# Kernel tuning notes

Measured on AMD Instinct MI355X. Metric: run time of the kernel, lower is better.

Reference implementation:

```python
import jax, jax.numpy as jnp
import numpy as np

S, B, E, H = 512, 128, 256, 256  # seq_len (nodes), num_samples, embb_dim, hidd_dim
CLIP = 10.0


def setup_inputs() -> dict:
    key = jax.random.key(0)
    ks = jax.random.split(key, 12)
    sc = 1.0 / np.sqrt(H)
    rn = lambda k, shape, s: (jax.random.normal(k, shape, dtype=jnp.float32) * s)
    x = rn(ks[0], (S, E), 1.0)
    # Gumbel noise for deterministic multinomial (Gumbel-argmax) sampling
    u = jax.random.uniform(ks[1], (S, B, S), minval=1e-6, maxval=1.0 - 1e-6)
    gumbel = -jnp.log(-jnp.log(u))
    return {
        "x": x,
        "gumbel": gumbel,
        "W_ih": rn(ks[2], (4 * H, E), sc),
        "W_hh": rn(ks[3], (4 * H, H), sc),
        "b_ih": jnp.zeros((4 * H,), jnp.float32),
        "b_hh": jnp.zeros((4 * H,), jnp.float32),
        "Wa_dec": rn(ks[4], (H, H), sc),
        "Wa_enc": rn(ks[5], (H, H), sc),
        "b_a": jnp.zeros((H,), jnp.float32),
        "v": rn(ks[6], (H,), sc),
        "init_dec": jnp.zeros((E,), jnp.float32),
        "num_samples": B,
    }


def _pointer_decode(x, gumbel, W_ih, W_hh, b_ih, b_hh, Wa_dec, Wa_enc, b_a, v,
                    init_dec, num_samples):
    Sn = x.shape[0]
    Bn = num_samples
    Hh = W_hh.shape[1]
    # encoder part of additive attention, computed once: [S, H]
    enc_proj = x @ Wa_enc.T + b_a

    h0 = jnp.zeros((Bn, Hh), x.dtype)
    c0 = jnp.zeros((Bn, Hh), x.dtype)
    dec0 = jnp.broadcast_to(init_dec, (Bn, init_dec.shape[0]))
    mask0 = jnp.ones((Bn, Sn), bool)
    lps0 = jnp.zeros((Bn,), x.dtype)
    ar = jnp.arange(Bn)

    def step(carry, g):
        h, c, di, m, lps = carry
        # single-layer LSTM cell (torch gate order: i, f, g, o)
        gates = di @ W_ih.T + b_ih + h @ W_hh.T + b_hh
        i_, f_, g_, o_ = jnp.split(gates, 4, axis=-1)
        c = jax.nn.sigmoid(f_) * c + jax.nn.sigmoid(i_) * jnp.tanh(g_)
        h = jax.nn.sigmoid(o_) * jnp.tanh(c)
        # additive attention: tanh(W [dec; enc] + b) . v, with logit clipping
        energy = jnp.tanh((h @ Wa_dec.T)[:, None, :] + enc_proj[None, :, :])  # [B,S,H]
        logits = CLIP * jnp.tanh(energy @ v)  # [B,S]
        logits = jnp.where(m, logits, -jnp.inf)
        lp = jax.nn.log_softmax(logits, axis=1)
        # multinomial sample via Gumbel-argmax over unmasked probs
        sel = jnp.argmax(lp + g, axis=1)  # [B]
        lps = lps + lp[ar, sel]
        di = x[sel]  # next decoder input = embedding of chosen node
        m = m.at[ar, sel].set(False)  # mask out chosen node
        return (h, c, di, m, lps), sel

    (_, _, _, _, log_probs_sum), sels = jax.lax.scan(
        step, (h0, c0, dec0, mask0, lps0), gumbel)
    predicted_mappings = sels.T  # [B, S]
    return predicted_mappings, log_probs_sum


def reference(x, gumbel, W_ih, W_hh, b_ih, b_hh, Wa_dec, Wa_enc, b_a, v,
              init_dec, num_samples):
    return _pointer_decode(x, gumbel, W_ih, W_hh, b_ih, b_hh, Wa_dec, Wa_enc,
                           b_a, v, init_dec, num_samples)
```

## Files before the change

kernel.cpp:

```cpp
#include <hip/hip_runtime.h>
#include <math.h>

#define SN 512
#define BN 128
#define HN 256
#define NSLICE 16
#define NGRP   16

#define B_EPT    ((size_t)0)
#define B_XPROJ  ((size_t)1048576)
#define B_IPROJ  ((size_t)5242880)
#define B_BIAS   ((size_t)5251072)
#define B_WIHT   ((size_t)5259264)
#define B_XT     ((size_t)6307840)
#define B_EX     ((size_t)6832128)
#define PAR_STRIDE 131072
#define EX_SLOTS  (2*PAR_STRIDE)

#define L_PB    0
#define L_PP3   36864
#define L_PF    73728
#define L_VLD   110592
#define L_HF    112640
#define L_HWF   129280
#define L_XPRO  145920
#define L_MASK  150016
#define L_CL    152064
#define L_BIAS  153088
#define L_SEL   153600
#define SMEM_TOTAL 153664

typedef double v2d __attribute__((ext_vector_type(2)));

#define TAGC 0x9E3779B97F4A7C15ULL
__device__ __forceinline__ long long d2ll(double d) { return __double_as_longlong(d); }

__device__ __forceinline__ double rcp64(double d) {
    double r;
    asm("v_rcp_f64 %0, %1" : "=v"(r) : "v"(d));
    r = __builtin_fma(__builtin_fma(-d, r, 1.0), r, r);
    r = __builtin_fma(__builtin_fma(-d, r, 1.0), r, r);
    return r;
}
__device__ __forceinline__ double rcp64f(double d) {
    double r;
    asm("v_rcp_f64 %0, %1" : "=v"(r) : "v"(d));
    r = __builtin_fma(__builtin_fma(-d, r, 1.0), r, r);
    return r;
}

__device__ __forceinline__ double exp2n(double t) {
    t = fmax(t, -1000.0);
    double n = __builtin_rint(t);
    double z = (t - n) * 0.69314718055994530942;
    double p = 2.5052108385441718775e-8;
    p = __builtin_fma(p, z, 2.7557319223985892511e-7);
    p = __builtin_fma(p, z, 2.7557319223985890653e-6);
    p = __builtin_fma(p, z, 2.4801587301587301566e-5);
    p = __builtin_fma(p, z, 1.9841269841269841253e-4);
    p = __builtin_fma(p, z, 1.3888888888888889419e-3);
    p = __builtin_fma(p, z, 8.3333333333333332177e-3);
    p = __builtin_fma(p, z, 4.1666666666666664354e-2);
    p = __builtin_fma(p, z, 1.6666666666666666574e-1);
    p = __builtin_fma(p, z, 0.5);
    p = __builtin_fma(p, z, 1.0);
    p = __builtin_fma(p, z, 1.0);
    long long ni = (long long)(int)n;
    return __longlong_as_double(__double_as_longlong(p) + (ni << 52));
}
__device__ __forceinline__ double tanh64(double x) {
    double a = fabs(x);
    double e = exp2n(a * -2.8853900817779268147);
    double r = rcp64(1.0 + e);
    return copysign((1.0 - e) * r, x);
}
__device__ __forceinline__ double sigmoid64(double g) {
    double a = fabs(g);
    double e = exp2n(a * -1.4426950408889634074);
    double r = rcp64(1.0 + e);
    double num = (g >= 0.0) ? 1.0 : e;
    return num * r;
}

__device__ __forceinline__ void pub16(double2* p, double v, unsigned long long tg) {
    v2d t2;
    t2.x = v;
    t2.y = __longlong_as_double(d2ll(v) ^ (long long)tg);
    asm volatile("global_store_dwordx4 %0, %1, off sc0 sc1" :: "v"(p), "v"(t2) : "memory");
}
__device__ __forceinline__ void gath2(const double2* p, unsigned long long tg,
                                      double* o0, double* o1) {
    v2d a, b;
    for (;;) {
        asm volatile("global_load_dwordx4 %0, %2, off sc0 sc1\n\t"
                     "global_load_dwordx4 %1, %2, off offset:16 sc0 sc1\n\t"
                     "s_waitcnt vmcnt(0)"
                     : "=&v"(a), "=&v"(b) : "v"(p) : "memory");
        bool ok = ((d2ll(a.x) ^ d2ll(a.y)) == (long long)tg) &
                  ((d2ll(b.x) ^ d2ll(b.y)) == (long long)tg);
        if (ok) break;
        __builtin_amdgcn_s_sleep(2);
    }
    *o0 = a.x; *o1 = b.x;
}

__global__ __launch_bounds__(256) void k_init_transpose(
    const float* __restrict__ Wih, const float* __restrict__ bih,
    const float* __restrict__ bhh, const float* __restrict__ x,
    float* __restrict__ ws)
{
    char* wsb = (char*)ws;
    float*  wiht = (float*)(wsb + B_WIHT);
    float*  xt   = (float*)(wsb + B_XT);
    double* bias = (double*)(wsb + B_BIAS);
    double2* ex  = (double2*)(wsb + B_EX);
    int i = blockIdx.x * 256 + threadIdx.x;
    if (i < 262144) {
        int e = i >> 10, r = i & 1023;
        wiht[i] = Wih[(size_t)r * 256 + e];
    } else if (i < 393216) {
        int j = i - 262144; int e = j >> 9, s = j & 511;
        xt[j] = x[(size_t)s * 256 + e];
    } else if (i < 394240) {
        int j = i - 393216;
        bias[j] = (double)bih[j] + (double)bhh[j];
    } else if (i < 394240 + EX_SLOTS) {
        double2 z; z.x = 0.0; z.y = 0.0;
        ex[i - 394240] = z;
    }
}

__global__ __launch_bounds__(512) void k_init_proj(
    const float* __restrict__ x, const float* __restrict__ Wae,
    const float* __restrict__ ba, const float* __restrict__ idec,
    float* __restrict__ ws)
{
    char* wsb = (char*)ws;
    const float* wiht = (const float*)(wsb + B_WIHT);
    const float* xt   = (const float*)(wsb + B_XT);
    double* ept   = (double*)(wsb + B_EPT);
    double* xproj = (double*)(wsb + B_XPROJ);
    double* iproj = (double*)(wsb + B_IPROJ);
    int blk = blockIdx.x, tid = threadIdx.x;
    if (blk < 256) {
        int k = blk, s = tid;
        double a = 0.0;
        for (int e = 0; e < 256; ++e)
            a += (double)Wae[(size_t)k * 256 + e] * (double)xt[(size_t)e * 512 + s];
        ept[(size_t)k * 512 + s] = tanh((double)ba[k] + a);
    } else if (blk < 256 + 1024) {
        int idx = blk - 256;
        int s = idx >> 1;
        int r = (idx & 1) * 512 + tid;
        double a = 0.0;
        for (int e = 0; e < 256; ++e)
            a += (double)x[(size_t)s * 256 + e] * (double)wiht[(size_t)e * 1024 + r];
        xproj[(size_t)s * 1024 + r] = a;
    } else {
        int r = (blk - 1280) * 512 + tid;
        double a = 0.0;
        for (int e = 0; e < 256; ++e)
            a += (double)idec[e] * (double)wiht[(size_t)e * 1024 + r];
        iproj[r] = a;
    }
}

__global__ __launch_bounds__(512, 2) void k_decode(
    const float* __restrict__ gmb, const float* __restrict__ vvec,
    const float* __restrict__ Whh, const float* __restrict__ Wad,
    float* __restrict__ ws, float* __restrict__ out)
{
    extern __shared__ char smem[];
    double* pb   = (double*)(smem + L_PB);
    double* pp3  = (double*)(smem + L_PP3);
    double* pf   = (double*)(smem + L_PF);
    double* vLd  = (double*)(smem + L_VLD);
    double* hf   = (double*)(smem + L_HF);
    double* hwf  = (double*)(smem + L_HWF);
    double* xpro = (double*)(smem + L_XPRO);
    double* mask = (double*)(smem + L_MASK);
    double* c_l  = (double*)(smem + L_CL);
    double* bias_l = (double*)(smem + L_BIAS);
    int*    selA = (int*)(smem + L_SEL);

    const int tid = threadIdx.x;
    const int g = blockIdx.x & 15;
    const int q = blockIdx.x >> 4;

    char* wsb = (char*)ws;
    const double* eptG   = (const double*)(wsb + B_EPT);
    const double* xprojG = (const double*)(wsb + B_XPROJ);
    const double* biasG  = (const double*)(wsb + B_BIAS);
    const double* iprojG = (const double*)(wsb + B_IPROJ);
    double2* exB = (double2*)(wsb + B_EX);

    for (int i = tid; i < 256; i += 512) vLd[i] = (double)vvec[i];
    if (tid < 64) bias_l[tid] = biasG[((tid >> 4) << 8) + q * 16 + (tid & 15)];
    for (int i = tid; i < 256; i += 512) mask[i] = 0.0;
    for (int i = tid; i < 128; i += 512) c_l[i] = 0.0;
    for (int i = tid; i < 2080; i += 512) { hf[i] = 0.0; hwf[i] = 0.0; }
    {
        int sl = tid >> 6, rl = tid & 63;
        int rg = ((rl >> 4) << 8) + q * 16 + (rl & 15);
        xpro[sl * 64 + rl] = iprojG[rg];
    }

    const int w = tid >> 6, lane = tid & 63;
    const int kc4 = tid >> 5, ss = tid & 31;

    double ev[16];
    #pragma unroll
    for (int kk = 0; kk < 16; ++kk)
        ev[kk] = eptG[(size_t)(kc4 * 16 + kk) * 512 + q * 32 + ss];
    const int rg1 = ((lane >> 4) << 8) + q * 16 + (lane & 15);
    const int kbase = w * 32;
    float wreg[32];
    {
        const float4* wrow = (const float4*)(Whh + (size_t)rg1 * 256 + kbase);
        #pragma unroll
        for (int j = 0; j < 8; ++j) {
            float4 v4 = wrow[j];
            wreg[4 * j + 0] = v4.x; wreg[4 * j + 1] = v4.y;
            wreg[4 * j + 2] = v4.z; wreg[4 * j + 3] = v4.w;
        }
    }
    float w3[8];
    {
        const float* wr3 = Wad + (size_t)(q * 16 + (tid & 15)) * 256 + (tid >> 4) * 8;
        #pragma unroll
        for (int kk = 0; kk < 8; ++kk) w3[kk] = wr3[kk];
    }
    __syncthreads();

    double lps = 0.0;

    for (int t = 0; t < SN; ++t) {
        const unsigned long long tg = (unsigned long long)(t + 2) * TAGC;
        double2* parB   = exB + (size_t)(t & 1) * PAR_STRIDE;
        double2* hexP   = parB + (size_t)g * 2048;
        double2* waexP  = parB + 32768 + (size_t)g * 2048;
        double2* lexP   = parB + 65536 + (size_t)g * 4096;

        float gv8[8];
        {
            const float* growW = gmb + (size_t)t * (BN * SN) + (size_t)(g * 8 + w) * SN;
            #pragma unroll
            for (int j = 0; j < 8; ++j)
                gv8[j] = __builtin_nontemporal_load(growW + lane + 64 * j);
        }

        #pragma unroll
        for (int slin = 0; slin < 4; ++slin) {
            int sl = slin;
            double a0 = 0.0, a1 = 0.0, a2 = 0.0, a3 = 0.0;
            #pragma unroll
            for (int g4 = 0; g4 < 8; ++g4) {
                const double* hp = hf + sl * 260 + kbase + 4 * g4;
                double2 hA = *(const double2*)(hp);
                double2 hB = *(const double2*)(hp + 2);
                a0 += (double)wreg[4 * g4 + 0] * hA.x;
                a1 += (double)wreg[4 * g4 + 1] * hA.y;
                a2 += (double)wreg[4 * g4 + 2] * hB.x;
                a3 += (double)wreg[4 * g4 + 3] * hB.y;
            }
            pb[w * 576 + lane * 9 + sl] = ((a0 + a1) + (a2 + a3));
        }
        __syncthreads();

        if (w == 0) {
            int jl = lane & 15, slin = lane >> 4;
            int sl = slin;
            double gvv[4];
            #pragma unroll
            for (int gate = 0; gate < 4; ++gate) {
                int rl = gate * 16 + jl;
                double p0 = pb[0 * 576 + rl * 9 + sl], p1 = pb[1 * 576 + rl * 9 + sl];
                double p2 = pb[2 * 576 + rl * 9 + sl], p3 = pb[3 * 576 + rl * 9 + sl];
                double p4 = pb[4 * 576 + rl * 9 + sl], p5 = pb[5 * 576 + rl * 9 + sl];
                double p6 = pb[6 * 576 + rl * 9 + sl], p7 = pb[7 * 576 + rl * 9 + sl];
                double s8 = ((p0 + p1) + (p2 + p3)) + ((p4 + p5) + (p6 + p7));
                gvv[gate] = bias_l[rl] + xpro[sl * 64 + rl] + s8;
            }
            double si = sigmoid64(gvv[0]);
            double sf = sigmoid64(gvv[1]);
            double so = sigmoid64(gvv[3]);
            double cf = sf * c_l[jl * 8 + sl] + si * tanh64(gvv[2]);
            double hn = so * tanh64(cf);
            c_l[jl * 8 + sl] = cf;
            pub16(&hexP[sl * 256 + q * 16 + jl], hn, tg);
        }

        #pragma unroll
        for (int slin = 0; slin < 4; ++slin) {
            int sl = 4 + slin;
            double a0 = 0.0, a1 = 0.0, a2 = 0.0, a3 = 0.0;
            #pragma unroll
            for (int g4 = 0; g4 < 8; ++g4) {
                const double* hp = hf + sl * 260 + kbase + 4 * g4;
                double2 hA = *(const double2*)(hp);
                double2 hB = *(const double2*)(hp + 2);
                a0 += (double)wreg[4 * g4 + 0] * hA.x;
                a1 += (double)wreg[4 * g4 + 1] * hA.y;
                a2 += (double)wreg[4 * g4 + 2] * hB.x;
                a3 += (double)wreg[4 * g4 + 3] * hB.y;
            }
            pb[w * 576 + lane * 9 + sl] = ((a0 + a1) + (a2 + a3));
        }
        __syncthreads();

        if (w == 1) {
            int jl = lane & 15, slin = lane >> 4;
            int sl = 4 + slin;
            double gvv[4];
            #pragma unroll
            for (int gate = 0; gate < 4; ++gate) {
                int rl = gate * 16 + jl;
                double p0 = pb[0 * 576 + rl * 9 + sl], p1 = pb[1 * 576 + rl * 9 + sl];
                double p2 = pb[2 * 576 + rl * 9 + sl], p3 = pb[3 * 576 + rl * 9 + sl];
                double p4 = pb[4 * 576 + rl * 9 + sl], p5 = pb[5 * 576 + rl * 9 + sl];
                double p6 = pb[6 * 576 + rl * 9 + sl], p7 = pb[7 * 576 + rl * 9 + sl];
                double s8 = ((p0 + p1) + (p2 + p3)) + ((p4 + p5) + (p6 + p7));
                gvv[gate] = bias_l[rl] + xpro[sl * 64 + rl] + s8;
            }
            double si = sigmoid64(gvv[0]);
            double sf = sigmoid64(gvv[1]);
            double so = sigmoid64(gvv[3]);
            double cf = sf * c_l[jl * 8 + sl] + si * tanh64(gvv[2]);
            double hn = so * tanh64(cf);
            c_l[jl * 8 + sl] = cf;
            pub16(&hexP[sl * 256 + q * 16 + jl], hn, tg);
        }

        {
            int sl = lane >> 4;
            int k  = kbase + (lane & 15) * 2;
            gath2(hexP + sl * 256 + k, tg, &hf[sl * 260 + k], &hf[sl * 260 + k + 1]);
        }

        {
            int kc = tid >> 4, rl = tid & 15;
            #pragma unroll
            for (int sl = 0; sl < 4; ++sl) {
                double a = 0.0;
                #pragma unroll
                for (int kk = 0; kk < 8; ++kk)
                    a += (double)w3[kk] * hf[sl * 260 + kc * 8 + kk];
                pp3[kc * 144 + rl * 9 + sl] = a;
            }
        }
        __syncthreads();
        if (w == 2) {
            int rl = lane & 15, slin = lane >> 4;
            int sl = slin;
            double s = 0.0;
            for (int kc = 0; kc < 32; ++kc) s += pp3[kc * 144 + rl * 9 + sl];
            pub16(&waexP[sl * 256 + q * 16 + rl], tanh64(s), tg);
        }

        {
            int sl = 4 + (lane >> 4);
            int k  = kbase + (lane & 15) * 2;
            gath2(hexP + sl * 256 + k, tg, &hf[sl * 260 + k], &hf[sl * 260 + k + 1]);
        }

        {
            int kc = tid >> 4, rl = tid & 15;
            #pragma unroll
            for (int slin = 0; slin < 4; ++slin) {
                int sl = 4 + slin;
                double a = 0.0;
                #pragma unroll
                for (int kk = 0; kk < 8; ++kk)
                    a += (double)w3[kk] * hf[sl * 260 + kc * 8 + kk];
                pp3[kc * 144 + rl * 9 + sl] = a;
            }
        }
        __syncthreads();
        if (w == 3) {
            int rl = lane & 15, slin = lane >> 4;
            int sl = 4 + slin;
            double s = 0.0;
            for (int kc = 0; kc < 32; ++kc) s += pp3[kc * 144 + rl * 9 + sl];
            pub16(&waexP[sl * 256 + q * 16 + rl], tanh64(s), tg);
        }

        {
            int sl = lane >> 4;
            int k  = kbase + (lane & 15) * 2;
            gath2(waexP + sl * 256 + k, tg, &hwf[sl * 260 + k], &hwf[sl * 260 + k + 1]);
        }

        {
            double vd[16];
            #pragma unroll
            for (int kk = 0; kk < 16; ++kk) vd[kk] = vLd[kc4 * 16 + kk];
            #pragma unroll 1
            for (int sl = 0; sl < 4; ++sl) {
                double a = 0.0;
                #pragma unroll
                for (int j = 0; j < 8; ++j) {
                    double2 h2 = *(const double2*)(hwf + sl * 260 + kc4 * 16 + 2 * j);
                    {
                        double Ta = ev[2 * j + 0], Tb = h2.x;
                        double d = __builtin_fma(Ta, Tb, 1.0);
                        double r = rcp64f(d);
                        a = __builtin_fma(vd[2 * j + 0], (Ta + Tb) * r, a);
                    }
                    {
                        double Ta = ev[2 * j + 1], Tb = h2.y;
                        double d = __builtin_fma(Ta, Tb, 1.0);
                        double r = rcp64f(d);
                        a = __builtin_fma(vd[2 * j + 1], (Ta + Tb) * r, a);
                    }
                }
                pf[kc4 * 288 + ss * 9 + sl] = a;
            }
        }
        __syncthreads();
        if (tid < 128) {
            int sA = tid & 31, slin = tid >> 5;
            int sl = slin;
            double u = 0.0;
            for (int kc = 0; kc < 16; ++kc) u += pf[kc * 288 + sA * 9 + sl];
            double lg = 10.0 * tanh64(u);
            pub16(&lexP[sl * 512 + q * 32 + sA], lg + mask[sA * 8 + sl], tg);
        }

        {
            int sl = 4 + (lane >> 4);
            int k  = kbase + (lane & 15) * 2;
            gath2(waexP + sl * 256 + k, tg, &hwf[sl * 260 + k], &hwf[sl * 260 + k + 1]);
        }

        {
            double vd[16];
            #pragma unroll
            for (int kk = 0; kk < 16; ++kk) vd[kk] = vLd[kc4 * 16 + kk];
            #pragma unroll 1
            for (int slin = 0; slin < 4; ++slin) {
                int sl = 4 + slin;
                double a = 0.0;
                #pragma unroll
                for (int j = 0; j < 8; ++j) {
                    double2 h2 = *(const double2*)(hwf + sl * 260 + kc4 * 16 + 2 * j);
                    {
                        double Ta = ev[2 * j + 0], Tb = h2.x;
                        double d = __builtin_fma(Ta, Tb, 1.0);
                        double r = rcp64f(d);
                        a = __builtin_fma(vd[2 * j + 0], (Ta + Tb) * r, a);
                    }
                    {
                        double Ta = ev[2 * j + 1], Tb = h2.y;
                        double d = __builtin_fma(Ta, Tb, 1.0);
                        double r = rcp64f(d);
                        a = __builtin_fma(vd[2 * j + 1], (Ta + Tb) * r, a);
                    }
                }
                pf[kc4 * 288 + ss * 9 + sl] = a;
            }
        }
        __syncthreads();
        if (tid < 128) {
            int sA = tid & 31, slin = tid >> 5;
            int sl = 4 + slin;
            double u = 0.0;
            for (int kc = 0; kc < 16; ++kc) u += pf[kc * 288 + sA * 9 + sl];
            double lg = 10.0 * tanh64(u);
            pub16(&lexP[sl * 512 + q * 32 + sA], lg + mask[sA * 8 + sl], tg);
        }

        {
            const double2* b0 = lexP + (size_t)w * 512 + lane;
            const double2* b1 = b0 + 256;
            double lv[8];
            for (;;) {
                v2d q0, q1, q2, q3, q4, q5, q6, q7;
                asm volatile(
                    "global_load_dwordx4 %0, %8, off sc0 sc1\n\t"
                    "global_load_dwordx4 %1, %8, off offset:1024 sc0 sc1\n\t"
                    "global_load_dwordx4 %2, %8, off offset:2048 sc0 sc1\n\t"
                    "global_load_dwordx4 %3, %8, off offset:3072 sc0 sc1\n\t"
                    "global_load_dwordx4 %4, %9, off sc0 sc1\n\t"
                    "global_load_dwordx4 %5, %9, off offset:1024 sc0 sc1\n\t"
                    "global_load_dwordx4 %6, %9, off offset:2048 sc0 sc1\n\t"
                    "global_load_dwordx4 %7, %9, off offset:3072 sc0 sc1\n\t"
                    "s_waitcnt vmcnt(0)"
                    : "=&v"(q0), "=&v"(q1), "=&v"(q2), "=&v"(q3),
                      "=&v"(q4), "=&v"(q5), "=&v"(q6), "=&v"(q7)
                    : "v"(b0), "v"(b1) : "memory");
                bool ok = ((d2ll(q0.x) ^ d2ll(q0.y)) == (long long)tg) &
                          ((d2ll(q1.x) ^ d2ll(q1.y)) == (long long)tg) &
                          ((d2ll(q2.x) ^ d2ll(q2.y)) == (long long)tg) &
                          ((d2ll(q3.x) ^ d2ll(q3.y)) == (long long)tg) &
                          ((d2ll(q4.x) ^ d2ll(q4.y)) == (long long)tg) &
                          ((d2ll(q5.x) ^ d2ll(q5.y)) == (long long)tg) &
                          ((d2ll(q6.x) ^ d2ll(q6.y)) == (long long)tg) &
                          ((d2ll(q7.x) ^ d2ll(q7.y)) == (long long)tg);
                if (ok) {
                    lv[0] = q0.x; lv[1] = q1.x; lv[2] = q2.x; lv[3] = q3.x;
                    lv[4] = q4.x; lv[5] = q5.x; lv[6] = q6.x; lv[7] = q7.x;
                    break;
                }
                __builtin_amdgcn_s_sleep(2);
            }
            double M = -INFINITY;
            #pragma unroll
            for (int j = 0; j < 8; ++j) M = fmax(M, lv[j]);
            #pragma unroll
            for (int off = 32; off >= 1; off >>= 1) M = fmax(M, __shfl_xor(M, off, 64));
            float se = 0.f;
            #pragma unroll
            for (int j = 0; j < 8; ++j) se += expf((float)(lv[j] - M));
            #pragma unroll
            for (int off = 32; off >= 1; off >>= 1) se += __shfl_xor(se, off, 64);
            float logS = logf(se);
            double best = -INFINITY; int bidx = 0x7fffffff; double bl = 0.0;
            #pragma unroll
            for (int j = 0; j < 8; ++j) {
                int s = lane + 64 * j;
                double cd = lv[j] + (double)gv8[j];
                if (cd > best || (cd == best && s < bidx)) { best = cd; bidx = s; bl = lv[j]; }
            }
            #pragma unroll
            for (int off = 32; off >= 1; off >>= 1) {
                double ob = __shfl_xor(best, off, 64);
                int    oi = __shfl_xor(bidx, off, 64);
                double ol = __shfl_xor(bl, off, 64);
                if (ob > best || (ob == best && oi < bidx)) { best = ob; bidx = oi; bl = ol; }
            }
            lps += (bl - M) - (double)logS;
            if (lane == 0) {
                selA[w] = bidx;
                if (q == 0) out[(size_t)(g * 8 + w) * SN + t] = (float)bidx;
            }
        }
        __syncthreads();
        if (tid < 256) {
            int sA = tid >> 3, sl = tid & 7;
            if (selA[sl] == q * 32 + sA) mask[sA * 8 + sl] = -INFINITY;
        }
        {
            int sl = tid >> 6, rl = tid & 63;
            int rg = ((rl >> 4) << 8) + q * 16 + (rl & 15);
            xpro[sl * 64 + rl] = xprojG[(size_t)selA[sl] * 1024 + rg];
        }
    }
    if (q == 0 && lane == 0) out[(size_t)BN * SN + g * 8 + w] = (float)lps;
}

extern "C" void kernel_launch(void* const* d_in, const int* in_sizes, int n_in,
                              void* d_out, int out_size, void* d_ws, size_t ws_size,
                              hipStream_t stream)
{
    const float* x    = (const float*)d_in[0];
    const float* gmb  = (const float*)d_in[1];
    const float* Wih  = (const float*)d_in[2];
    const float* Whh  = (const float*)d_in[3];
    const float* bih  = (const float*)d_in[4];
    const float* bhh  = (const float*)d_in[5];
    const float* Wad  = (const float*)d_in[6];
    const float* Wae  = (const float*)d_in[7];
    const float* ba   = (const float*)d_in[8];
    const float* vvec = (const float*)d_in[9];
    const float* idec = (const float*)d_in[10];
    float* ws = (float*)d_ws;
    float* out = (float*)d_out;

    hipFuncSetAttribute(reinterpret_cast<const void*>(k_decode),
                        hipFuncAttributeMaxDynamicSharedMemorySize, SMEM_TOTAL);

    hipLaunchKernelGGL(k_init_transpose, dim3(2564), dim3(256), 0, stream,
                       Wih, bih, bhh, x, ws);
    hipLaunchKernelGGL(k_init_proj, dim3(1282), dim3(512), 0, stream,
                       x, Wae, ba, idec, ws);
    hipLaunchKernelGGL(k_decode, dim3(256), dim3(512), SMEM_TOTAL, stream,
                       gmb, vvec, Whh, Wad, ws, out);
}
```

Baseline: 8.885 ms.

## Merge half-batch phases and overlap next-step recurrent matvec with logit exchange

Drops the split of each step into two half-batch passes per stage (LSTM gates, Wa_dec projection, attention energy), so each stage now handles all 8 local samples at once with fewer block barriers and global exchange rounds. The W_hh·h partial products for the next step are now computed right after the logits are published, overlapping the wait on other blocks' logits, and pb is zero-initialised so the first step sees h=0. Spin-wait sleep shrinks to the minimum. The cost is that the old overlap between the two halves is lost, and polling becomes more aggressive.

Result: slower. 9.520 ms (+7.2%).

```diff
diff --git a/kernel.cpp b/kernel.cpp
--- a/kernel.cpp
+++ b/kernel.cpp
@@ -15,7 +15,7 @@
 #define B_XT     ((size_t)6307840)
 #define B_EX     ((size_t)6832128)
 #define PAR_STRIDE 131072
-#define EX_SLOTS  (2*PAR_STRIDE)
+#define EX_TOTAL  (2*PAR_STRIDE)
 
 #define L_PB    0
 #define L_PP3   36864
@@ -96,10 +96,9 @@
                      "global_load_dwordx4 %1, %2, off offset:16 sc0 sc1\n\t"
                      "s_waitcnt vmcnt(0)"
                      : "=&v"(a), "=&v"(b) : "v"(p) : "memory");
-        bool ok = ((d2ll(a.x) ^ d2ll(a.y)) == (long long)tg) &
-                  ((d2ll(b.x) ^ d2ll(b.y)) == (long long)tg);
-        if (ok) break;
-        __builtin_amdgcn_s_sleep(2);
+        if (((d2ll(a.x) ^ d2ll(a.y)) == (long long)tg) &
+            ((d2ll(b.x) ^ d2ll(b.y)) == (long long)tg)) break;
+        __builtin_amdgcn_s_sleep(1);
     }
     *o0 = a.x; *o1 = b.x;
 }
@@ -124,7 +123,7 @@
     } else if (i < 394240) {
         int j = i - 393216;
         bias[j] = (double)bih[j] + (double)bhh[j];
-    } else if (i < 394240 + EX_SLOTS) {
+    } else if (i < 394240 + EX_TOTAL) {
         double2 z; z.x = 0.0; z.y = 0.0;
         ex[i - 394240] = z;
     }
@@ -199,6 +198,7 @@
     for (int i = tid; i < 256; i += 512) mask[i] = 0.0;
     for (int i = tid; i < 128; i += 512) c_l[i] = 0.0;
     for (int i = tid; i < 2080; i += 512) { hf[i] = 0.0; hwf[i] = 0.0; }
+    for (int i = tid; i < 4608; i += 512) pb[i] = 0.0;
     {
         int sl = tid >> 6, rl = tid & 63;
         int rg = ((rl >> 4) << 8) + q * 16 + (rl & 15);
@@ -241,6 +241,8 @@
         double2* waexP  = parB + 32768 + (size_t)g * 2048;
         double2* lexP   = parB + 65536 + (size_t)g * 4096;
 
+        __syncthreads();
+
         float gv8[8];
         {
             const float* growW = gmb + (size_t)t * (BN * SN) + (size_t)(g * 8 + w) * SN;
@@ -249,27 +251,9 @@
                 gv8[j] = __builtin_nontemporal_load(growW + lane + 64 * j);
         }
 
-        #pragma unroll
-        for (int slin = 0; slin < 4; ++slin) {
-            int sl = slin;
-            double a0 = 0.0, a1 = 0.0, a2 = 0.0, a3 = 0.0;
-            #pragma unroll
-            for (int g4 = 0; g4 < 8; ++g4) {
-                const double* hp = hf + sl * 260 + kbase + 4 * g4;
-                double2 hA = *(const double2*)(hp);
-                double2 hB = *(const double2*)(hp + 2);
-                a0 += (double)wreg[4 * g4 + 0] * hA.x;
-                a1 += (double)wreg[4 * g4 + 1] * hA.y;
-                a2 += (double)wreg[4 * g4 + 2] * hB.x;
-                a3 += (double)wreg[4 * g4 + 3] * hB.y;
-            }
-            pb[w * 576 + lane * 9 + sl] = ((a0 + a1) + (a2 + a3));
-        }
-        __syncthreads();
-
-        if (w == 0) {
+        if (w < 2) {
             int jl = lane & 15, slin = lane >> 4;
-            int sl = slin;
+            int sl = w * 4 + slin;
             double gvv[4];
             #pragma unroll
             for (int gate = 0; gate < 4; ++gate) {
@@ -290,57 +274,18 @@
             pub16(&hexP[sl * 256 + q * 16 + jl], hn, tg);
         }
 
-        #pragma unroll
-        for (int slin = 0; slin < 4; ++slin) {
-            int sl = 4 + slin;
-            double a0 = 0.0, a1 = 0.0, a2 = 0.0, a3 = 0.0;
-            #pragma unroll
-            for (int g4 = 0; g4 < 8; ++g4) {
-                const double* hp = hf + sl * 260 + kbase + 4 * g4;
-                double2 hA = *(const double2*)(hp);
-                double2 hB = *(const double2*)(hp + 2);
-                a0 += (double)wreg[4 * g4 + 0] * hA.x;
-                a1 += (double)wreg[4 * g4 + 1] * hA.y;
-                a2 += (double)wreg[4 * g4 + 2] * hB.x;
-                a3 += (double)wreg[4 * g4 + 3] * hB.y;
-            }
-            pb[w * 576 + lane * 9 + sl] = ((a0 + a1) + (a2 + a3));
-        }
-        __syncthreads();
-
-        if (w == 1) {
-            int jl = lane & 15, slin = lane >> 4;
-            int sl = 4 + slin;
-            double gvv[4];
-            #pragma unroll
-            for (int gate = 0; gate < 4; ++gate) {
-                int rl = gate * 16 + jl;
-                double p0 = pb[0 * 576 + rl * 9 + sl], p1 = pb[1 * 576 + rl * 9 + sl];
-                double p2 = pb[2 * 576 + rl * 9 + sl], p3 = pb[3 * 576 + rl * 9 + sl];
-                double p4 = pb[4 * 576 + rl * 9 + sl], p5 = pb[5 * 576 + rl * 9 + sl];
-                double p6 = pb[6 * 576 + rl * 9 + sl], p7 = pb[7 * 576 + rl * 9 + sl];
-                double s8 = ((p0 + p1) + (p2 + p3)) + ((p4 + p5) + (p6 + p7));
-                gvv[gate] = bias_l[rl] + xpro[sl * 64 + rl] + s8;
-            }
-            double si = sigmoid64(gvv[0]);
-            double sf = sigmoid64(gvv[1]);
-            double so = sigmoid64(gvv[3]);
-            double cf = sf * c_l[jl * 8 + sl] + si * tanh64(gvv[2]);
-            double hn = so * tanh64(cf);
-            c_l[jl * 8 + sl] = cf;
-            pub16(&hexP[sl * 256 + q * 16 + jl], hn, tg);
-        }
-
         {
             int sl = lane >> 4;
             int k  = kbase + (lane & 15) * 2;
             gath2(hexP + sl * 256 + k, tg, &hf[sl * 260 + k], &hf[sl * 260 + k + 1]);
+            int sl2 = sl + 4;
+            gath2(hexP + sl2 * 256 + k, tg, &hf[sl2 * 260 + k], &hf[sl2 * 260 + k + 1]);
         }
 
         {
             int kc = tid >> 4, rl = tid & 15;
             #pragma unroll
-            for (int sl = 0; sl < 4; ++sl) {
+            for (int sl = 0; sl < 8; ++sl) {
                 double a = 0.0;
                 #pragma unroll
                 for (int kk = 0; kk < 8; ++kk)
@@ -349,45 +294,20 @@
             }
         }
         __syncthreads();
-        if (w == 2) {
+        if (w == 2 || w == 3) {
             int rl = lane & 15, slin = lane >> 4;
-            int sl = slin;
+            int sl = (w - 2) * 4 + slin;
             double s = 0.0;
             for (int kc = 0; kc < 32; ++kc) s += pp3[kc * 144 + rl * 9 + sl];
             pub16(&waexP[sl * 256 + q * 16 + rl], tanh64(s), tg);
         }
 
         {
-            int sl = 4 + (lane >> 4);
-            int k  = kbase + (lane & 15) * 2;
-            gath2(hexP + sl * 256 + k, tg, &hf[sl * 260 + k], &hf[sl * 260 + k + 1]);
-        }
-
-        {
-            int kc = tid >> 4, rl = tid & 15;
-            #pragma unroll
-            for (int slin = 0; slin < 4; ++slin) {
-                int sl = 4 + slin;
-                double a = 0.0;
-                #pragma unroll
-                for (int kk = 0; kk < 8; ++kk)
-                    a += (double)w3[kk] * hf[sl * 260 + kc * 8 + kk];
-                pp3[kc * 144 + rl * 9 + sl] = a;
-            }
-        }
-        __syncthreads();
-        if (w == 3) {
-            int rl = lane & 15, slin = lane >> 4;
-            int sl = 4 + slin;
-            double s = 0.0;
-            for (int kc = 0; kc < 32; ++kc) s += pp3[kc * 144 + rl * 9 + sl];
-            pub16(&waexP[sl * 256 + q * 16 + rl], tanh64(s), tg);
-        }
-
-        {
             int sl = lane >> 4;
             int k  = kbase + (lane & 15) * 2;
             gath2(waexP + sl * 256 + k, tg, &hwf[sl * 260 + k], &hwf[sl * 260 + k + 1]);
+            int sl2 = sl + 4;
+            gath2(waexP + sl2 * 256 + k, tg, &hwf[sl2 * 260 + k], &hwf[sl2 * 260 + k + 1]);
         }
 
         {
@@ -395,7 +315,7 @@
             #pragma unroll
             for (int kk = 0; kk < 16; ++kk) vd[kk] = vLd[kc4 * 16 + kk];
             #pragma unroll 1
-            for (int sl = 0; sl < 4; ++sl) {
+            for (int sl = 0; sl < 8; ++sl) {
                 double a = 0.0;
                 #pragma unroll
                 for (int j = 0; j < 8; ++j) {
@@ -417,56 +337,28 @@
             }
         }
         __syncthreads();
-        if (tid < 128) {
-            int sA = tid & 31, slin = tid >> 5;
-            int sl = slin;
+        if (tid < 256) {
+            int sA = tid & 31, sl = tid >> 5;
             double u = 0.0;
             for (int kc = 0; kc < 16; ++kc) u += pf[kc * 288 + sA * 9 + sl];
             double lg = 10.0 * tanh64(u);
             pub16(&lexP[sl * 512 + q * 32 + sA], lg + mask[sA * 8 + sl], tg);
         }
 
-        {
-            int sl = 4 + (lane >> 4);
-            int k  = kbase + (lane & 15) * 2;
-            gath2(waexP + sl * 256 + k, tg, &hwf[sl * 260 + k], &hwf[sl * 260 + k + 1]);
-        }
-
-        {
-            double vd[16];
-            #pragma unroll
-            for (int kk = 0; kk < 16; ++kk) vd[kk] = vLd[kc4 * 16 + kk];
-            #pragma unroll 1
-            for (int slin = 0; slin < 4; ++slin) {
-                int sl = 4 + slin;
-                double a = 0.0;
-                #pragma unroll
-                for (int j = 0; j < 8; ++j) {
-                    double2 h2 = *(const double2*)(hwf + sl * 260 + kc4 * 16 + 2 * j);
-                    {
-                        double Ta = ev[2 * j + 0], Tb = h2.x;
-                        double d = __builtin_fma(Ta, Tb, 1.0);
-                        double r = rcp64f(d);
-                        a = __builtin_fma(vd[2 * j + 0], (Ta + Tb) * r, a);
-                    }
-                    {
-                        double Ta = ev[2 * j + 1], Tb = h2.y;
-                        double d = __builtin_fma(Ta, Tb, 1.0);
-                        double r = rcp64f(d);
-                        a = __builtin_fma(vd[2 * j + 1], (Ta + Tb) * r, a);
-                    }
-                }
-                pf[kc4 * 288 + ss * 9 + sl] = a;
-            }
-        }
-        __syncthreads();
-        if (tid < 128) {
-            int sA = tid & 31, slin = tid >> 5;
-            int sl = 4 + slin;
-            double u = 0.0;
-            for (int kc = 0; kc < 16; ++kc) u += pf[kc * 288 + sA * 9 + sl];
-            double lg = 10.0 * tanh64(u);
-            pub16(&lexP[sl * 512 + q * 32 + sA], lg + mask[sA * 8 + sl], tg);
+        #pragma unroll
+        for (int sl = 0; sl < 8; ++sl) {
+            double a0 = 0.0, a1 = 0.0, a2 = 0.0, a3 = 0.0;
+            #pragma unroll
+            for (int g4 = 0; g4 < 8; ++g4) {
+                const double* hp = hf + sl * 260 + kbase + 4 * g4;
+                double2 hA = *(const double2*)(hp);
+                double2 hB = *(const double2*)(hp + 2);
+                a0 += (double)wreg[4 * g4 + 0] * hA.x;
+                a1 += (double)wreg[4 * g4 + 1] * hA.y;
+                a2 += (double)wreg[4 * g4 + 2] * hB.x;
+                a3 += (double)wreg[4 * g4 + 3] * hB.y;
+            }
+            pb[w * 576 + lane * 9 + sl] = ((a0 + a1) + (a2 + a3));
         }
 
         {
@@ -501,7 +393,7 @@
                     lv[4] = q4.x; lv[5] = q5.x; lv[6] = q6.x; lv[7] = q7.x;
                     break;
                 }
-                __builtin_amdgcn_s_sleep(2);
+                __builtin_amdgcn_s_sleep(1);
             }
             double M = -INFINITY;
             #pragma unroll
```
